# Optimization experiments

Hardware: AMD Instinct MI355X
Metric: run time of the kernel (lower is better)

The kernel has to match this reference:

```python
import jax, jax.numpy as jnp
import numpy as np

H = 16        # num attention heads
KVH = 4       # num key/value heads
D = 128       # head dim
WIN = 1024    # sliding window (in packed per-state positions)
THETA = 10000.0
NUM_STATES = 8


def rotate_half(x):
    half = x.shape[-1] // 2
    return jnp.concatenate([-x[..., half:], x[..., :half]], axis=-1)


def setup_inputs() -> dict:
    key = jax.random.key(0)
    ks = jax.random.split(key, 6)
    B, L, HID = 2, 2048, 2048
    s = 0.02
    hidden_states = jax.random.normal(ks[0], (B, L, HID), jnp.float32)
    Wq = jax.random.normal(ks[1], (H * D, HID), jnp.float32) * s
    Wk = jax.random.normal(ks[2], (KVH * D, HID), jnp.float32) * s
    Wv = jax.random.normal(ks[3], (KVH * D, HID), jnp.float32) * s
    Wo = jax.random.normal(ks[4], (HID, H * D), jnp.float32) * s
    sid = jax.random.randint(ks[5], (B, L), 0, NUM_STATES).astype(jnp.int64)
    position_ids = jnp.tile(jnp.arange(L, dtype=jnp.int64)[None, :], (B, 1))
    return dict(hidden_states=hidden_states, Wq=Wq, Wk=Wk, Wv=Wv, Wo=Wo,
                sid=sid, position_ids=position_ids)


def reference(hidden_states, Wq, Wk, Wv, Wo, sid, position_ids):
    B, L, HID = hidden_states.shape
    # projections (Linear without bias: x @ W.T)
    q = (hidden_states @ Wq.T).reshape(B, L, H, D)
    k = (hidden_states @ Wk.T).reshape(B, L, KVH, D)
    v = (hidden_states @ Wv.T).reshape(B, L, KVH, D)
    # rotary embedding
    inv_freq = 1.0 / (THETA ** (jnp.arange(0, D, 2, dtype=jnp.float32) / D))
    freqs = position_ids.astype(jnp.float32)[:, :, None] * inv_freq[None, None, :]  # [B,L,D/2]
    emb = jnp.concatenate([freqs, freqs], axis=-1)                                  # [B,L,D]
    cos = jnp.cos(emb)[:, :, None, :].astype(hidden_states.dtype)
    sin = jnp.sin(emb)[:, :, None, :].astype(hidden_states.dtype)
    q = q * cos + rotate_half(q) * sin
    k = k * cos + rotate_half(k) * sin
    # GQA: repeat kv heads (repeat_interleave along head dim)
    n_rep = H // KVH
    k = jnp.repeat(k, n_rep, axis=2)  # [B,L,H,D]
    v = jnp.repeat(v, n_rep, axis=2)
    # BoSs mask: attend within same state id, causal, sliding window over
    # packed-per-state rank distance (equivalent to the varlen packing path)
    same = sid[:, :, None] == sid[:, None, :]                  # [B,L,L]
    tril = jnp.tril(jnp.ones((L, L), dtype=bool))[None]        # [1,L,L]
    rank = jnp.sum(same & tril, axis=-1) - 1                   # [B,L] rank within own state
    win_ok = (rank[:, :, None] - rank[:, None, :]) <= WIN
    mask = same & tril & win_ok                                # [B,L,L]
    scale = D ** -0.5
    scores = jnp.einsum('bqhd,bkhd->bhqk', q, k) * scale       # [B,H,L,L]
    scores = jnp.where(mask[:, None, :, :], scores, jnp.finfo(scores.dtype).min)
    attn = jax.nn.softmax(scores, axis=-1)
    o = jnp.einsum('bhqk,bkhd->bqhd', attn, v).reshape(B, L, H * D)
    return o @ Wo.T
```

## Files before the change

### kernel.cpp

```cpp
#include <hip/hip_runtime.h>
#include <hip/hip_bf16.h>

#define H_ 16
#define KVH_ 4
#define D_ 128
#define L_ 2048
#define B_ 2
#define HID_ 2048
#define WIN_ 1024
#define NS_ 8
#define QKV_N 3072

typedef __attribute__((ext_vector_type(8))) short short8;
typedef __attribute__((ext_vector_type(4))) float floatx4;

__device__ inline float bf16_to_f(unsigned short u) {
    union { unsigned int i; float f; } c; c.i = ((unsigned int)u) << 16; return c.f;
}
__device__ inline unsigned short f_to_bf16(float f) {
    __hip_bfloat16 h = __float2bfloat16(f);
    return *(unsigned short*)&h;
}

__device__ inline int world_is_bf16(const unsigned short* hs_u) {
    int lane = threadIdx.x & 63;
    unsigned short u = hs_u[(lane & 31) * 2];
    int e = (u >> 7) & 0xFF;
    unsigned long long bad = __ballot(e > 130);
    return bad == 0ULL;
}
__device__ inline int pid_stride(const int* pids) { return (pids[1] == 0) ? 2 : 1; }

__global__ __launch_bounds__(256) void convert_all(const void* __restrict__ hs,
                                                   const void* __restrict__ Wq,
                                                   const void* __restrict__ Wk,
                                                   const void* __restrict__ Wv,
                                                   const void* __restrict__ Wo,
                                                   unsigned short* __restrict__ c_hs,
                                                   unsigned short* __restrict__ c_Wq,
                                                   unsigned short* __restrict__ c_Wk,
                                                   unsigned short* __restrict__ c_Wv,
                                                   unsigned short* __restrict__ c_Wo) {
    int isbf = world_is_bf16((const unsigned short*)hs);
    const int N0 = (B_ * L_ * HID_) / 4;
    const int N1 = (HID_ * HID_) / 4;
    const int N2 = (KVH_ * D_ * HID_) / 4;
    const int N3 = N2;
    const int N4 = N1;
    const int total = N0 + N1 + N2 + N3 + N4;
    for (int i = blockIdx.x * 256 + threadIdx.x; i < total; i += gridDim.x * 256) {
        int j = i;
        const void* src; unsigned short* dst;
        if (j < N0)              { src = hs; dst = c_hs; }
        else if ((j -= N0) < N1) { src = Wq; dst = c_Wq; }
        else if ((j -= N1) < N2) { src = Wk; dst = c_Wk; }
        else if ((j -= N2) < N3) { src = Wv; dst = c_Wv; }
        else                     { j -= N3; src = Wo; dst = c_Wo; }
        if (isbf) {
            ((ushort4*)dst)[j] = ((const ushort4*)src)[j];
        } else {
            float4 f = ((const float4*)src)[j];
            ushort4 o4;
            o4.x = f_to_bf16(f.x); o4.y = f_to_bf16(f.y);
            o4.z = f_to_bf16(f.z); o4.w = f_to_bf16(f.w);
            ((ushort4*)dst)[j] = o4;
        }
    }
}

__global__ __launch_bounds__(256) void scan_kernel(const int* __restrict__ sid,
                                                   const int* __restrict__ pids,
                                                   int* __restrict__ rank,
                                                   int* __restrict__ poslist,
                                                   int* __restrict__ counts) {
    int stride = pid_stride(pids);
    int b = blockIdx.x;
    int t = threadIdx.x;
    __shared__ int cnt[256][NS_];
    __shared__ int pre[256][NS_];
    const int* s = sid + (size_t)b * L_ * stride;
    int myid[8];
#pragma unroll
    for (int i = 0; i < 8; i++) myid[i] = s[(t * 8 + i) * stride];
#pragma unroll
    for (int st = 0; st < NS_; st++) cnt[t][st] = 0;
#pragma unroll
    for (int i = 0; i < 8; i++) cnt[t][myid[i]]++;
    __syncthreads();
    for (int off = 1; off < 256; off <<= 1) {
        int add[NS_];
        if (t >= off)
#pragma unroll
            for (int st = 0; st < NS_; st++) add[st] = cnt[t - off][st];
        __syncthreads();
        if (t >= off)
#pragma unroll
            for (int st = 0; st < NS_; st++) cnt[t][st] += add[st];
        __syncthreads();
    }
#pragma unroll
    for (int st = 0; st < NS_; st++) pre[t][st] = t ? cnt[t - 1][st] : 0;
    if (t == 255)
#pragma unroll
        for (int st = 0; st < NS_; st++) counts[b * NS_ + st] = cnt[255][st];
    __syncthreads();
#pragma unroll
    for (int i = 0; i < 8; i++) {
        int sd = myid[i];
        int r = pre[t][sd]++;
        int pos = t * 8 + i;
        rank[b * L_ + pos] = r;
        poslist[((size_t)b * NS_ + sd) * L_ + r] = pos;
    }
}

#define STAGE(gptr, ldsdst)                                                     \
    __builtin_amdgcn_global_load_lds(                                           \
        (const __attribute__((address_space(1))) unsigned int*)(gptr),          \
        (__attribute__((address_space(3))) unsigned int*)(ldsdst), 16, 0, 0)

#define READ_A(MH, KK)                                                          \
    _Pragma("unroll")                                                           \
    for (int mt = 0; mt < 4; ++mt)                                              \
        af[mt] = *(const short8*)&Ab[(arow + (MH) * 64 + mt * 16) * 64          \
                                     + ((((KK) << 2) | quad) ^ axor) * 8]

#define READ_B(KK)                                                              \
    _Pragma("unroll")                                                           \
    for (int nt = 0; nt < 4; ++nt)                                              \
        bf[nt] = *(const short8*)&Bb[(brr + nt * 16) * 64                       \
                                     + ((((KK) << 2) | quad) ^ axor) * 8]

#define MFMA_H(MH)                                                              \
    __builtin_amdgcn_s_setprio(1);                                              \
    _Pragma("unroll")                                                           \
    for (int mt = 0; mt < 4; ++mt)                                              \
        _Pragma("unroll")                                                       \
        for (int nt = 0; nt < 4; ++nt)                                          \
            acc[(MH) * 4 + mt][nt] = __builtin_amdgcn_mfma_f32_16x16x32_bf16(   \
                af[mt], bf[nt], acc[(MH) * 4 + mt][nt], 0, 0, 0);               \
    __builtin_amdgcn_s_setprio(0)

#define LGKM0_PIN() do {                                                        \
    asm volatile("s_waitcnt lgkmcnt(0)" ::: "memory");                          \
    __builtin_amdgcn_sched_barrier(0); } while (0)

#define VM2_BAR() do {                                                          \
    asm volatile("s_waitcnt vmcnt(2)" ::: "memory");                            \
    __builtin_amdgcn_s_barrier();                                               \
    asm volatile("" ::: "memory"); } while (0)

__global__ __launch_bounds__(512, 1) void gemm256(const unsigned short* __restrict__ A,
                                                  const unsigned short* __restrict__ B0,
                                                  const unsigned short* __restrict__ B1,
                                                  const unsigned short* __restrict__ B2,
                                                  void* __restrict__ C,
                                                  int M, int N, int K,
                                                  int nb1, int nb2,
                                                  const unsigned short* __restrict__ hs_probe,
                                                  int c_mode) {
    __shared__ unsigned short As[2][16384];
    __shared__ unsigned short Bs[2][16384];
    int tid = threadIdx.x;
    int wave = tid >> 6, lane = tid & 63;
    int quad = lane >> 4, l16 = lane & 15;
    int wr = wave >> 2, wc = wave & 3;
    int bn_t = blockIdx.x;
    int bm = blockIdx.y * 256, bn = bn_t * 256;

    const unsigned short* Bseg;
    int brow0;
    if (bn_t < nb1)      { Bseg = B0; brow0 = bn; }
    else if (bn_t < nb2) { Bseg = B1; brow0 = bn - nb1 * 256; }
    else                 { Bseg = B2; brow0 = bn - nb2 * 256; }

    int sub = tid >> 3, slot = tid & 7;
    int swz = slot ^ (sub & 7);
    unsigned int a_off[4], b_off[4];
#pragma unroll
    for (int c = 0; c < 4; ++c) {
        a_off[c] = (unsigned int)((bm + c * 64 + sub) * K + swz * 8);
        b_off[c] = (unsigned int)((brow0 + c * 64 + sub) * K + swz * 8);
    }

    const int arow = wr * 128 + l16;
    const int brr  = wc * 64 + l16;
    const int axor = l16 & 7;

    floatx4 acc[8][4] = {};
    short8 af[4], bf[4];
    const int KT = K >> 6;

    STAGE(Bseg + b_off[0], &Bs[0][0 * 4096 + tid * 8]);
    STAGE(Bseg + b_off[1], &Bs[0][1 * 4096 + tid * 8]);
    STAGE(Bseg + b_off[2], &Bs[0][2 * 4096 + tid * 8]);
    STAGE(Bseg + b_off[3], &Bs[0][3 * 4096 + tid * 8]);
    STAGE(A + a_off[0], &As[0][0 * 4096 + tid * 8]);
    STAGE(A + a_off[2], &As[0][2 * 4096 + tid * 8]);
    STAGE(A + a_off[1], &As[0][1 * 4096 + tid * 8]);
    STAGE(A + a_off[3], &As[0][3 * 4096 + tid * 8]);

    for (int t = 0; t < KT; ++t) {
        const unsigned short* Ab = As[t & 1];
        const unsigned short* Bb = Bs[t & 1];
        unsigned short* AsN = As[(t & 1) ^ 1];
        unsigned short* BsN = Bs[(t & 1) ^ 1];
        int tn = (t + 1 < KT) ? t + 1 : t;
        unsigned int kel = (unsigned int)tn * 64;

        VM2_BAR();
        READ_A(0, 0);
        READ_B(0);
        STAGE(Bseg + b_off[0] + kel, &BsN[0 * 4096 + tid * 8]);
        STAGE(Bseg + b_off[1] + kel, &BsN[1 * 4096 + tid * 8]);
        LGKM0_PIN();
        MFMA_H(0);

        VM2_BAR();
        READ_A(1, 0);
        STAGE(Bseg + b_off[2] + kel, &BsN[2 * 4096 + tid * 8]);
        STAGE(Bseg + b_off[3] + kel, &BsN[3 * 4096 + tid * 8]);
        LGKM0_PIN();
        MFMA_H(1);

        READ_A(0, 1);
        READ_B(1);
        STAGE(A + a_off[0] + kel, &AsN[0 * 4096 + tid * 8]);
        STAGE(A + a_off[2] + kel, &AsN[2 * 4096 + tid * 8]);
        LGKM0_PIN();
        MFMA_H(0);

        READ_A(1, 1);
        STAGE(A + a_off[1] + kel, &AsN[1 * 4096 + tid * 8]);
        STAGE(A + a_off[3] + kel, &AsN[3 * 4096 + tid * 8]);
        LGKM0_PIN();
        MFMA_H(1);
    }
    asm volatile("s_waitcnt vmcnt(0)" ::: "memory");

    int cf32 = c_mode ? !world_is_bf16(hs_probe) : 0;
#pragma unroll
    for (int a = 0; a < 8; ++a)
#pragma unroll
        for (int g = 0; g < 4; ++g)
#pragma unroll
            for (int r = 0; r < 4; ++r) {
                int row = bm + wr * 128 + (a >> 2) * 64 + (a & 3) * 16 + quad * 4 + r;
                int col = bn + wc * 64 + g * 16 + l16;
                size_t idx = (size_t)row * N + col;
                if (cf32) ((float*)C)[idx] = acc[a][g][r];
                else      ((unsigned short*)C)[idx] = f_to_bf16(acc[a][g][r]);
            }
}

__global__ __launch_bounds__(256) void rope_kernel(unsigned short* __restrict__ qkv,
                                                   const int* __restrict__ pos_ids) {
    int stride = pid_stride(pos_ids);
    int idx = blockIdx.x * 256 + threadIdx.x;
    int i = idx & 63;
    int tmp = idx >> 6;
    int head = tmp % 20;
    int bl = tmp / 20;
    if (bl >= B_ * L_) return;
    float posf = (float)pos_ids[bl * stride];
    float inv = exp2f(-(float)i * (2.0f / 128.0f) * 13.287712379549449f);
    float ang = posf * inv;
    float c = cosf(ang), sn = sinf(ang);
    unsigned short* p = qkv + (size_t)bl * QKV_N +
                        ((head < H_) ? head * D_ : 2048 + (head - H_) * D_);
    float x0 = bf16_to_f(p[i]), x1 = bf16_to_f(p[i + 64]);
    p[i]      = f_to_bf16(x0 * c - x1 * sn);
    p[i + 64] = f_to_bf16(x1 * c + x0 * sn);
}

__global__ __launch_bounds__(256, 4) void attn_mfma(const unsigned short* __restrict__ qkv,
                                                    const int* __restrict__ counts,
                                                    const int* __restrict__ poslist,
                                                    unsigned short* __restrict__ o) {
    int qt  = blockIdx.x & 127;
    int kvh = (blockIdx.x >> 7) & 3;
    int s   = (blockIdx.x >> 9) & 7;
    int b   = blockIdx.x >> 12;
    int n = counts[b * NS_ + s];
    if (qt * 16 >= n) return;
    const int* plist = poslist + ((size_t)b * NS_ + s) * L_;

    __shared__ short Ksh[32][136];
    __shared__ short Vsh[128][40];
    __shared__ short Psh[4][16][40];
    __shared__ int posq[16];

    int tid = threadIdx.x;
    int wave = tid >> 6, lane = tid & 63;
    int quad = lane >> 4, l16 = lane & 15;
    int h = kvh * 4 + wave;
    const float scale = 0.08838834764831845f;

    if (tid < 16) posq[tid] = plist[min(qt * 16 + tid, n - 1)];
    __syncthreads();

    short8 qf[4];
    {
        const unsigned short* gq =
            qkv + ((size_t)(b << 11) + posq[l16]) * QKV_N + h * D_;
#pragma unroll
        for (int kk = 0; kk < 4; kk++)
            qf[kk] = *(const short8*)(gq + kk * 32 + quad * 8);
    }

    float m_r[4], l_r[4];
    floatx4 Ov[8];
#pragma unroll
    for (int r4 = 0; r4 < 4; r4++) { m_r[r4] = -1e30f; l_r[r4] = 0.f; }
#pragma unroll
    for (int nt = 0; nt < 8; nt++) Ov[nt] = (floatx4){0.f, 0.f, 0.f, 0.f};

    int c0 = max(0, (qt * 16 - WIN_) >> 5);
    int nch = ((qt * 16 + 15) >> 5) + 1;

    int r = tid >> 3, seg = tid & 7;
    int vc = r ^ ((seg & 3) << 3);
    short8 kr0, kr1, vr0, vr1;
    {
        int kpos = plist[min(c0 * 32 + r, n - 1)];
        size_t base = ((size_t)(b << 11) + kpos) * QKV_N + 2048 + kvh * D_ + seg * 16;
        kr0 = *(const short8*)(qkv + base);
        kr1 = *(const short8*)(qkv + base + 8);
        vr0 = *(const short8*)(qkv + base + 512);
        vr1 = *(const short8*)(qkv + base + 520);
    }

    for (int c = c0; c < nch; c++) {
        *(short8*)&Ksh[r][seg * 16]     = kr0;
        *(short8*)&Ksh[r][seg * 16 + 8] = kr1;
#pragma unroll
        for (int e = 0; e < 8; e++) Vsh[seg * 16 + e][vc] = vr0[e];
#pragma unroll
        for (int e = 0; e < 8; e++) Vsh[seg * 16 + 8 + e][vc] = vr1[e];
        __syncthreads();

        if (c + 1 < nch) {
            int kpos = plist[min((c + 1) * 32 + r, n - 1)];
            size_t base = ((size_t)(b << 11) + kpos) * QKV_N + 2048 + kvh * D_ + seg * 16;
            kr0 = *(const short8*)(qkv + base);
            kr1 = *(const short8*)(qkv + base + 8);
            vr0 = *(const short8*)(qkv + base + 512);
            vr1 = *(const short8*)(qkv + base + 520);
        }

        floatx4 s0 = (floatx4){0.f, 0.f, 0.f, 0.f};
        floatx4 s1 = (floatx4){0.f, 0.f, 0.f, 0.f};
#pragma unroll
        for (int kk = 0; kk < 4; kk++) {
            short8 kfa = *(const short8*)&Ksh[l16][kk * 32 + quad * 8];
            s0 = __builtin_amdgcn_mfma_f32_16x16x32_bf16(qf[kk], kfa, s0, 0, 0, 0);
        }
#pragma unroll
        for (int kk = 0; kk < 4; kk++) {
            short8 kfb = *(const short8*)&Ksh[16 + l16][kk * 32 + quad * 8];
            s1 = __builtin_amdgcn_mfma_f32_16x16x32_bf16(qf[kk], kfb, s1, 0, 0, 0);
        }

        int kr0i = c * 32 + l16, kr1i = kr0i + 16;
        float x0[4], x1[4], rmax[4];
#pragma unroll
        for (int r4 = 0; r4 < 4; r4++) {
            int qr = qt * 16 + quad * 4 + r4;
            bool mk0 = (kr0i <= qr) && (kr0i >= qr - WIN_);
            bool mk1 = (kr1i <= qr) && (kr1i >= qr - WIN_);
            x0[r4] = mk0 ? s0[r4] * scale : -1e30f;
            x1[r4] = mk1 ? s1[r4] * scale : -1e30f;
            rmax[r4] = fmaxf(x0[r4], x1[r4]);
        }
#pragma unroll
        for (int st = 1; st <= 8; st <<= 1)
#pragma unroll
            for (int r4 = 0; r4 < 4; r4++)
                rmax[r4] = fmaxf(rmax[r4], __shfl_xor(rmax[r4], st, 64));
        float al[4], psum[4];
#pragma unroll
        for (int r4 = 0; r4 < 4; r4++) {
            float nm = fmaxf(m_r[r4], rmax[r4]);
            al[r4] = __expf(m_r[r4] - nm);
            m_r[r4] = nm;
            x0[r4] = (x0[r4] > -1e29f) ? __expf(x0[r4] - nm) : 0.f;
            x1[r4] = (x1[r4] > -1e29f) ? __expf(x1[r4] - nm) : 0.f;
            psum[r4] = x0[r4] + x1[r4];
        }
#pragma unroll
        for (int st = 1; st <= 8; st <<= 1)
#pragma unroll
            for (int r4 = 0; r4 < 4; r4++)
                psum[r4] += __shfl_xor(psum[r4], st, 64);
#pragma unroll
        for (int r4 = 0; r4 < 4; r4++) l_r[r4] = l_r[r4] * al[r4] + psum[r4];
#pragma unroll
        for (int nt = 0; nt < 8; nt++)
#pragma unroll
            for (int r4 = 0; r4 < 4; r4++) Ov[nt][r4] *= al[r4];

#pragma unroll
        for (int r4 = 0; r4 < 4; r4++) {
            Psh[wave][quad * 4 + r4][l16]      = (short)f_to_bf16(x0[r4]);
            Psh[wave][quad * 4 + r4][16 + l16] = (short)f_to_bf16(x1[r4]);
        }
        short8 pf = *(const short8*)&Psh[wave][l16][quad * 8];

#pragma unroll
        for (int nt = 0; nt < 8; nt++) {
            short8 vf = *(const short8*)&Vsh[nt * 16 + l16][(quad ^ (nt & 3)) * 8];
            Ov[nt] = __builtin_amdgcn_mfma_f32_16x16x32_bf16(pf, vf, Ov[nt], 0, 0, 0);
        }
        __syncthreads();
    }

    float inv_r[4];
    int pos_r[4], qvalid[4];
#pragma unroll
    for (int r4 = 0; r4 < 4; r4++) {
        int qr = qt * 16 + quad * 4 + r4;
        qvalid[r4] = (qr < n);
        inv_r[r4] = 1.f / l_r[r4];
        pos_r[r4] = posq[quad * 4 + r4];
    }
#pragma unroll
    for (int nt = 0; nt < 8; nt++)
#pragma unroll
        for (int r4 = 0; r4 < 4; r4++)
            if (qvalid[r4])
                o[(((size_t)(b << 11) + pos_r[r4]) * H_ + h) * D_ + nt * 16 + l16] =
                    f_to_bf16(Ov[nt][r4] * inv_r[r4]);
}

extern "C" void kernel_launch(void* const* d_in, const int* in_sizes, int n_in,
                              void* d_out, int out_size, void* d_ws, size_t ws_size,
                              hipStream_t stream) {
    const void* hs = d_in[0];
    const void* Wq = d_in[1];
    const void* Wk = d_in[2];
    const void* Wv = d_in[3];
    const void* Wo = d_in[4];
    const int* sid  = (const int*)d_in[5];
    const int* pids = (const int*)d_in[6];

    const int M = B_ * L_;
    char* w = (char*)d_ws;
    unsigned short* qkv  = (unsigned short*)(w + 256);
    unsigned short* o_b  = (unsigned short*)(w + 25166080);
    unsigned short* c_hs = (unsigned short*)(w + 41943296);
    unsigned short* c_Wq = (unsigned short*)(w + 58720512);
    unsigned short* c_Wk = (unsigned short*)(w + 67109120);
    unsigned short* c_Wv = (unsigned short*)(w + 69206272);
    unsigned short* c_Wo = (unsigned short*)(w + 71303424);
    int* rank            = (int*)(w + 79692032);
    int* plist           = (int*)(w + 79708416);
    int* counts          = (int*)(w + 79839488);

    const unsigned short* hs_probe = (const unsigned short*)hs;

    convert_all<<<2048, 256, 0, stream>>>(hs, Wq, Wk, Wv, Wo,
                                          c_hs, c_Wq, c_Wk, c_Wv, c_Wo);

    scan_kernel<<<B_, 256, 0, stream>>>(sid, pids, rank, plist, counts);

    gemm256<<<dim3(QKV_N / 256, M / 256), 512, 0, stream>>>(
        c_hs, c_Wq, c_Wk, c_Wv, qkv, M, QKV_N, HID_, 8, 10, hs_probe, 0);

    int rope_threads = M * (H_ + KVH_) * 64;
    rope_kernel<<<(rope_threads + 255) / 256, 256, 0, stream>>>(qkv, pids);

    attn_mfma<<<B_ * NS_ * KVH_ * (L_ / 16), 256, 0, stream>>>(qkv, counts, plist, o_b);

    gemm256<<<dim3(HID_ / 256, M / 256), 512, 0, stream>>>(
        o_b, c_Wo, c_Wo, c_Wo, d_out, M, HID_, HID_, 1 << 30, 1 << 30, hs_probe, 1);
}
```

Baseline: 313.8 us.

## Template GEMM on M-tile height and restructure K-loop with double register fragments

The GEMM is templated on M tile size. The output projection now uses 128x256 tiles, so it launches twice as many workgroups (256 instead of 128) and fills more of the chip's compute units. The inner K loop is reorganised: it takes one full vmcnt(0) barrier per iteration instead of two vmcnt(2) barriers. It also uses two sets of A/B register fragments, so LDS reads for the next k-subtile can overlap the MFMAs, with sched barriers controlling the ordering. The costs are more registers and waiting for all outstanding loads at each barrier, which may expose more global load latency.

```diff
diff --git a/kernel.cpp b/kernel.cpp
--- a/kernel.cpp
+++ b/kernel.cpp
@@ -119,54 +119,48 @@
         (const __attribute__((address_space(1))) unsigned int*)(gptr),          \
         (__attribute__((address_space(3))) unsigned int*)(ldsdst), 16, 0, 0)
 
-#define READ_A(MH, KK)                                                          \
+#define SB __builtin_amdgcn_sched_barrier(0)
+
+#define RD_A(dst, MH, KK)                                                       \
     _Pragma("unroll")                                                           \
-    for (int mt = 0; mt < 4; ++mt)                                              \
-        af[mt] = *(const short8*)&Ab[(arow + (MH) * 64 + mt * 16) * 64          \
-                                     + ((((KK) << 2) | quad) ^ axor) * 8]
-
-#define READ_B(KK)                                                              \
+    for (int mt = 0; mt < MT; ++mt)                                             \
+        dst[mt] = *(const short8*)&Ab[(arow + (MH) * (MT * 16) + mt * 16) * 64  \
+                                      + ((((KK) << 2) | quad) ^ axor) * 8]
+
+#define RD_B(dst, KK)                                                           \
     _Pragma("unroll")                                                           \
     for (int nt = 0; nt < 4; ++nt)                                              \
-        bf[nt] = *(const short8*)&Bb[(brr + nt * 16) * 64                       \
-                                     + ((((KK) << 2) | quad) ^ axor) * 8]
-
-#define MFMA_H(MH)                                                              \
+        dst[nt] = *(const short8*)&Bb[(brr + nt * 16) * 64                      \
+                                      + ((((KK) << 2) | quad) ^ axor) * 8]
+
+#define MFMA_C(AV, BV, MH)                                                      \
     __builtin_amdgcn_s_setprio(1);                                              \
     _Pragma("unroll")                                                           \
-    for (int mt = 0; mt < 4; ++mt)                                              \
+    for (int mt = 0; mt < MT; ++mt)                                             \
         _Pragma("unroll")                                                       \
         for (int nt = 0; nt < 4; ++nt)                                          \
-            acc[(MH) * 4 + mt][nt] = __builtin_amdgcn_mfma_f32_16x16x32_bf16(   \
-                af[mt], bf[nt], acc[(MH) * 4 + mt][nt], 0, 0, 0);               \
+            acc[(MH) * MT + mt][nt] = __builtin_amdgcn_mfma_f32_16x16x32_bf16(  \
+                AV[mt], BV[nt], acc[(MH) * MT + mt][nt], 0, 0, 0);              \
     __builtin_amdgcn_s_setprio(0)
 
-#define LGKM0_PIN() do {                                                        \
-    asm volatile("s_waitcnt lgkmcnt(0)" ::: "memory");                          \
-    __builtin_amdgcn_sched_barrier(0); } while (0)
-
-#define VM2_BAR() do {                                                          \
-    asm volatile("s_waitcnt vmcnt(2)" ::: "memory");                            \
-    __builtin_amdgcn_s_barrier();                                               \
-    asm volatile("" ::: "memory"); } while (0)
-
-__global__ __launch_bounds__(512, 1) void gemm256(const unsigned short* __restrict__ A,
-                                                  const unsigned short* __restrict__ B0,
-                                                  const unsigned short* __restrict__ B1,
-                                                  const unsigned short* __restrict__ B2,
-                                                  void* __restrict__ C,
-                                                  int M, int N, int K,
-                                                  int nb1, int nb2,
-                                                  const unsigned short* __restrict__ hs_probe,
-                                                  int c_mode) {
-    __shared__ unsigned short As[2][16384];
+template<int MT>
+__global__ __launch_bounds__(512, 1) void gemm_t(const unsigned short* __restrict__ A,
+                                                 const unsigned short* __restrict__ B0,
+                                                 const unsigned short* __restrict__ B1,
+                                                 const unsigned short* __restrict__ B2,
+                                                 void* __restrict__ C,
+                                                 int M, int N, int K,
+                                                 int nb1, int nb2,
+                                                 const unsigned short* __restrict__ hs_probe,
+                                                 int c_mode) {
+    __shared__ unsigned short As[2][MT * 4096];
     __shared__ unsigned short Bs[2][16384];
     int tid = threadIdx.x;
     int wave = tid >> 6, lane = tid & 63;
     int quad = lane >> 4, l16 = lane & 15;
     int wr = wave >> 2, wc = wave & 3;
     int bn_t = blockIdx.x;
-    int bm = blockIdx.y * 256, bn = bn_t * 256;
+    int bm = blockIdx.y * (MT * 64), bn = bn_t * 256;
 
     const unsigned short* Bseg;
     int brow0;
@@ -176,29 +170,26 @@
 
     int sub = tid >> 3, slot = tid & 7;
     int swz = slot ^ (sub & 7);
-    unsigned int a_off[4], b_off[4];
-#pragma unroll
-    for (int c = 0; c < 4; ++c) {
+    unsigned int a_off[MT], b_off[4];
+#pragma unroll
+    for (int c = 0; c < MT; ++c)
         a_off[c] = (unsigned int)((bm + c * 64 + sub) * K + swz * 8);
+#pragma unroll
+    for (int c = 0; c < 4; ++c)
         b_off[c] = (unsigned int)((brow0 + c * 64 + sub) * K + swz * 8);
-    }
-
-    const int arow = wr * 128 + l16;
+
+    const int arow = wr * (MT * 32) + l16;
     const int brr  = wc * 64 + l16;
     const int axor = l16 & 7;
 
-    floatx4 acc[8][4] = {};
-    short8 af[4], bf[4];
+    floatx4 acc[2 * MT][4] = {};
+    short8 a0[MT], a1[MT], b0[4], b1[4];
     const int KT = K >> 6;
 
-    STAGE(Bseg + b_off[0], &Bs[0][0 * 4096 + tid * 8]);
-    STAGE(Bseg + b_off[1], &Bs[0][1 * 4096 + tid * 8]);
-    STAGE(Bseg + b_off[2], &Bs[0][2 * 4096 + tid * 8]);
-    STAGE(Bseg + b_off[3], &Bs[0][3 * 4096 + tid * 8]);
-    STAGE(A + a_off[0], &As[0][0 * 4096 + tid * 8]);
-    STAGE(A + a_off[2], &As[0][2 * 4096 + tid * 8]);
-    STAGE(A + a_off[1], &As[0][1 * 4096 + tid * 8]);
-    STAGE(A + a_off[3], &As[0][3 * 4096 + tid * 8]);
+#pragma unroll
+    for (int c = 0; c < 4; ++c)  STAGE(Bseg + b_off[c], &Bs[0][c * 4096 + tid * 8]);
+#pragma unroll
+    for (int c = 0; c < MT; ++c) STAGE(A + a_off[c], &As[0][c * 4096 + tid * 8]);
 
     for (int t = 0; t < KT; ++t) {
         const unsigned short* Ab = As[t & 1];
@@ -208,44 +199,44 @@
         int tn = (t + 1 < KT) ? t + 1 : t;
         unsigned int kel = (unsigned int)tn * 64;
 
-        VM2_BAR();
-        READ_A(0, 0);
-        READ_B(0);
-        STAGE(Bseg + b_off[0] + kel, &BsN[0 * 4096 + tid * 8]);
-        STAGE(Bseg + b_off[1] + kel, &BsN[1 * 4096 + tid * 8]);
-        LGKM0_PIN();
-        MFMA_H(0);
-
-        VM2_BAR();
-        READ_A(1, 0);
-        STAGE(Bseg + b_off[2] + kel, &BsN[2 * 4096 + tid * 8]);
-        STAGE(Bseg + b_off[3] + kel, &BsN[3 * 4096 + tid * 8]);
-        LGKM0_PIN();
-        MFMA_H(1);
-
-        READ_A(0, 1);
-        READ_B(1);
-        STAGE(A + a_off[0] + kel, &AsN[0 * 4096 + tid * 8]);
-        STAGE(A + a_off[2] + kel, &AsN[2 * 4096 + tid * 8]);
-        LGKM0_PIN();
-        MFMA_H(0);
-
-        READ_A(1, 1);
-        STAGE(A + a_off[1] + kel, &AsN[1 * 4096 + tid * 8]);
-        STAGE(A + a_off[3] + kel, &AsN[3 * 4096 + tid * 8]);
-        LGKM0_PIN();
-        MFMA_H(1);
+        asm volatile("s_waitcnt vmcnt(0)" ::: "memory");
+        __builtin_amdgcn_s_barrier();
+        asm volatile("" ::: "memory");
+
+        RD_A(a0, 0, 0);
+        RD_B(b0, 0);
+        RD_A(a1, 1, 0);
+#pragma unroll
+        for (int c = 0; c < 4; ++c)
+            STAGE(Bseg + b_off[c] + kel, &BsN[c * 4096 + tid * 8]);
+        SB;
+        MFMA_C(a0, b0, 0);
+        SB;
+        RD_A(a0, 0, 1);
+        RD_B(b1, 1);
+#pragma unroll
+        for (int c = 0; c < MT; ++c)
+            STAGE(A + a_off[c] + kel, &AsN[c * 4096 + tid * 8]);
+        SB;
+        MFMA_C(a1, b0, 1);
+        SB;
+        RD_A(a1, 1, 1);
+        SB;
+        MFMA_C(a0, b1, 0);
+        SB;
+        MFMA_C(a1, b1, 1);
     }
     asm volatile("s_waitcnt vmcnt(0)" ::: "memory");
 
     int cf32 = c_mode ? !world_is_bf16(hs_probe) : 0;
 #pragma unroll
-    for (int a = 0; a < 8; ++a)
+    for (int a = 0; a < 2 * MT; ++a)
 #pragma unroll
         for (int g = 0; g < 4; ++g)
 #pragma unroll
             for (int r = 0; r < 4; ++r) {
-                int row = bm + wr * 128 + (a >> 2) * 64 + (a & 3) * 16 + quad * 4 + r;
+                int row = bm + wr * (MT * 32) + (a / MT) * (MT * 16)
+                        + (a % MT) * 16 + quad * 4 + r;
                 int col = bn + wc * 64 + g * 16 + l16;
                 size_t idx = (size_t)row * N + col;
                 if (cf32) ((float*)C)[idx] = acc[a][g][r];
@@ -463,7 +454,7 @@
 
     scan_kernel<<<B_, 256, 0, stream>>>(sid, pids, rank, plist, counts);
 
-    gemm256<<<dim3(QKV_N / 256, M / 256), 512, 0, stream>>>(
+    gemm_t<4><<<dim3(QKV_N / 256, M / 256), 512, 0, stream>>>(
         c_hs, c_Wq, c_Wk, c_Wv, qkv, M, QKV_N, HID_, 8, 10, hs_probe, 0);
 
     int rope_threads = M * (H_ + KVH_) * 64;
@@ -471,6 +462,6 @@
 
     attn_mfma<<<B_ * NS_ * KVH_ * (L_ / 16), 256, 0, stream>>>(qkv, counts, plist, o_b);
 
-    gemm256<<<dim3(HID_ / 256, M / 256), 512, 0, stream>>>(
+    gemm_t<2><<<dim3(HID_ / 256, M / 128), 512, 0, stream>>>(
         o_b, c_Wo, c_Wo, c_Wo, d_out, M, HID_, HID_, 1 << 30, 1 << 30, hs_probe, 1);
 }
```

Measured after the change: 300.3 us. 1.04x faster.
